# Kernel tuning notes

Measured on AMD Instinct MI355X. Metric: run time of the kernel, lower is better.

The kernel has to match this reference:

```python
import jax, jax.numpy as jnp
import numpy as np

B, N, F, FE, H, C = 2, 2048, 128, 8, 4, 64
LEAKY_ALPHA = 0.2
NEG_INF = -1e9


def setup_inputs() -> dict:
    key = jax.random.key(0)
    ks = jax.random.split(key, 8)
    return {
        "X": jax.random.normal(ks[0], (B, N, F), jnp.float32),
        "A": jax.random.uniform(ks[1], (B, N, N), jnp.float32),
        "E": jax.random.normal(ks[2], (B, N, N, FE), jnp.float32),
        "W_edge": jax.random.normal(ks[3], (FE, 1), jnp.float32) * 0.1,
        "b_edge": jnp.zeros((1,), jnp.float32),
        "W_gat": jax.random.normal(ks[4], (H, F, C), jnp.float32) * 0.05,
        "a_src": jax.random.normal(ks[5], (H, C), jnp.float32) * 0.1,
        "a_dst": jax.random.normal(ks[6], (H, C), jnp.float32) * 0.1,
        "b_gat": jnp.zeros((H * C,), jnp.float32),
        "ln_gamma": jnp.ones((H * C,), jnp.float32),
        "ln_beta": jnp.zeros((H * C,), jnp.float32),
    }


def reference(X, A, E, W_edge, b_edge, W_gat, a_src, a_dst, b_gat, ln_gamma, ln_beta):
    # --- edge gate: sigmoid(Dense_1(E)) -> [B,N,N], multiply into adjacency ---
    edge_w = jax.nn.sigmoid(jnp.einsum("bije,eo->bijo", E, W_edge) + b_edge)
    A = A * edge_w[..., 0]  # [B,N,N]

    # --- multi-head dense GAT (spektral GATConv, concat_heads, elu) ---
    h = jnp.einsum("bnf,hfc->bnhc", X, W_gat)  # [B,N,H,C]
    s_src = jnp.einsum("bnhc,hc->bnh", h, a_src)  # [B,N,H]
    s_dst = jnp.einsum("bnhc,hc->bnh", h, a_dst)
    # e_ij = LeakyReLU(src_i + dst_j): [B,N(i),N(j),H]
    logits = jax.nn.leaky_relu(s_src[:, :, None, :] + s_dst[:, None, :, :],
                               negative_slope=LEAKY_ALPHA)
    mask = jnp.where(A == 0.0, NEG_INF, 0.0)[..., None]  # [B,N,N,1]
    attn = jax.nn.softmax(logits + mask, axis=2)  # softmax over neighbors j
    out = jnp.einsum("bijh,bjhc->bihc", attn, h)  # [B,N,H,C]
    out = out.reshape(B, N, H * C) + b_gat
    out = jax.nn.elu(out)

    # --- LayerNorm over the feature axis (inference: dropout is identity) ---
    mu = jnp.mean(out, axis=-1, keepdims=True)
    var = jnp.var(out, axis=-1, keepdims=True)
    out = (out - mu) * jax.lax.rsqrt(var + 1e-3) * ln_gamma + ln_beta
    return out
```

## Files before the change

### kernel.cpp

```cpp
#include <hip/hip_runtime.h>
#include <hip/hip_bf16.h>


#define BB 2
#define NN 2048
#define FF 128
#define HH 4
#define CC 64
#define HC 256
#define TN 8
#define LOG2E 1.4426950408889634f

typedef __attribute__((ext_vector_type(8))) short short8;
typedef __attribute__((ext_vector_type(4))) float f32x4;

__device__ __forceinline__ float wave_sum(float v) {
#pragma unroll
    for (int m = 32; m >= 1; m >>= 1) v += __shfl_xor(v, m, 64);
    return v;
}

__device__ __forceinline__ unsigned short bf16rne(float x) {
    unsigned u = __float_as_uint(x);
    return (unsigned short)((u + 0x7fffu + ((u >> 16) & 1u)) >> 16);
}

__global__ __launch_bounds__(256) void k1_proj(
    const float* __restrict__ X, const float* __restrict__ Adj,
    const float* __restrict__ Wg,
    const float* __restrict__ a_src, const float* __restrict__ a_dst,
    unsigned short* __restrict__ hT, float* __restrict__ ssT,
    float* __restrict__ sdT, unsigned char* __restrict__ zT)
{
    __shared__ float sX[TN][FF];
    const int blk = blockIdx.x;
    const int b  = blk / (NN / TN);
    const int n0 = (blk % (NN / TN)) * TN;
    const int tid = threadIdx.x;
    const int h = tid >> 6, c = tid & 63;

    for (int idx = tid; idx < TN * FF; idx += 256) {
        int r = idx >> 7, f = idx & 127;
        sX[r][f] = X[(size_t)(b * NN + n0 + r) * FF + f];
    }
    __syncthreads();

    float hv[TN];
#pragma unroll
    for (int r = 0; r < TN; ++r) hv[r] = 0.f;

#pragma unroll 4
    for (int f4 = 0; f4 < FF / 4; ++f4) {
        const int f = f4 * 4;
        const float w0 = Wg[(h * FF + f + 0) * CC + c];
        const float w1 = Wg[(h * FF + f + 1) * CC + c];
        const float w2 = Wg[(h * FF + f + 2) * CC + c];
        const float w3 = Wg[(h * FF + f + 3) * CC + c];
#pragma unroll
        for (int r = 0; r < TN; ++r) {
            float4 x4 = *(const float4*)&sX[r][f];
            hv[r] = fmaf(x4.x, w0, hv[r]);
            hv[r] = fmaf(x4.y, w1, hv[r]);
            hv[r] = fmaf(x4.z, w2, hv[r]);
            hv[r] = fmaf(x4.w, w3, hv[r]);
        }
    }

    union { short8 v; unsigned short u[8]; } pk;
#pragma unroll
    for (int r = 0; r < TN; ++r) pk.u[r] = bf16rne(hv[r]);
    *(short8*)&hT[((size_t)(b * HH + h) * CC + c) * NN + n0] = pk.v;

    const float as = a_src[tid];
    const float ad = a_dst[tid];
#pragma unroll
    for (int r = 0; r < TN; ++r) {
        const int n = n0 + r;
        float s1 = wave_sum(hv[r] * as);
        float s2 = wave_sum(hv[r] * ad);
        if (c == 0) {
            ssT[(b * HH + h) * NN + n] = s1 * LOG2E;
            sdT[(b * HH + h) * NN + n] = s2 * LOG2E;
        }
    }

    {
        const int r = tid >> 5;
        const int s = tid & 31;
        const size_t row = (size_t)(b * NN + n0 + r);
        const float* ap = Adj + row * NN + s * 64;
        unsigned char* zp = zT + (row << 8);
#pragma unroll
        for (int k = 0; k < 8; ++k) {
            float4 a0 = *(const float4*)(ap + k * 8);
            float4 a1 = *(const float4*)(ap + k * 8 + 4);
            unsigned m = 0u;
            m |= (a0.x == 0.f) ? 1u   : 0u;
            m |= (a0.y == 0.f) ? 2u   : 0u;
            m |= (a0.z == 0.f) ? 4u   : 0u;
            m |= (a0.w == 0.f) ? 8u   : 0u;
            m |= (a1.x == 0.f) ? 16u  : 0u;
            m |= (a1.y == 0.f) ? 32u  : 0u;
            m |= (a1.z == 0.f) ? 64u  : 0u;
            m |= (a1.w == 0.f) ? 128u : 0u;
            const int jb = s * 8 + k;
            const int jq = jb >> 6, rem = jb & 63;
            const int it = rem >> 2, lq = rem & 3;
            zp[jq * 64 + lq * 16 + it] = (unsigned char)m;
        }
    }
}

struct Stage {
    float4 sda, sdb;
    short8 bfr[4];
};

__device__ __forceinline__ void load_stage(
    Stage& s, const float* sdp, const unsigned short* const* hb, int js)
{
    s.sda = *(const float4*)(sdp + js);
    s.sdb = *(const float4*)(sdp + js + 4);
#pragma unroll
    for (int ni = 0; ni < 4; ++ni) s.bfr[ni] = *(const short8*)(hb[ni] + js);
}

__device__ __forceinline__ void consume_stage(
    const Stage& s, float ss, unsigned mb, float& lsum, f32x4* acc)
{
    const float sd[8] = {s.sda.x, s.sda.y, s.sda.z, s.sda.w,
                         s.sdb.x, s.sdb.y, s.sdb.z, s.sdb.w};
    float p[8];
#pragma unroll
    for (int t = 0; t < 8; ++t) {
        float x = ss + sd[t];
        x = fmaxf(x, 0.2f * x);
        p[t] = __builtin_amdgcn_exp2f(x);
    }
    if (mb) {
#pragma unroll
        for (int t = 0; t < 8; ++t)
            if ((mb >> t) & 1u) p[t] = 0.f;
    }
#pragma unroll
    for (int t = 0; t < 8; ++t) lsum += p[t];

    union { short8 v; __hip_bfloat162 h2[4]; } pk;
#pragma unroll
    for (int t = 0; t < 4; ++t)
        pk.h2[t] = __float22bfloat162_rn(make_float2(p[2 * t], p[2 * t + 1]));
#pragma unroll
    for (int ni = 0; ni < 4; ++ni)
        acc[ni] = __builtin_amdgcn_mfma_f32_16x16x32_bf16(pk.v, s.bfr[ni], acc[ni], 0, 0, 0);
}

__global__ __launch_bounds__(1024, 4) void k2_attn(
    const unsigned short* __restrict__ hT, const float* __restrict__ ssT,
    const float* __restrict__ sdT, const unsigned char* __restrict__ zT,
    const float* __restrict__ b_gat, const float* __restrict__ gamma,
    const float* __restrict__ beta, float* __restrict__ out)
{
    __shared__ float accs[3][16][HH][64];
    __shared__ float lsumx[3][HH][16];
    __shared__ float red1s[HH][16], red2s[HH][16];

    const int blk = blockIdx.x;
    const int b  = blk >> 7;
    const int i0 = (blk & 127) << 4;
    const int tid  = threadIdx.x;
    const int wave = tid >> 6;
    const int h  = wave & 3;
    const int jq = wave >> 2;
    const int l  = tid & 63;
    const int lr = l & 15;
    const int lq = l >> 4;

    const float ss = ssT[(b * HH + h) * NN + i0 + lr];

    const uint4 mw = *(const uint4*)(zT + ((size_t)(b * NN + i0 + lr) << 8)
                                       + jq * 64 + lq * 16);
    const unsigned long long mlo = ((unsigned long long)mw.y << 32) | mw.x;
    const unsigned long long mhi = ((unsigned long long)mw.w << 32) | mw.z;

    f32x4 acc[4];
#pragma unroll
    for (int ni = 0; ni < 4; ++ni) acc[ni] = (f32x4){0.f, 0.f, 0.f, 0.f};
    float lsum = 0.f;

    const float* sdp  = sdT + (b * HH + h) * NN + jq * 512 + lq * 8;
    const unsigned short* hb[4];
#pragma unroll
    for (int ni = 0; ni < 4; ++ni)
        hb[ni] = hT + ((size_t)(b * HH + h) * CC + ni * 16 + lr) * NN + jq * 512 + lq * 8;

    Stage s0, s1;
    load_stage(s0, sdp, hb, 0);
#pragma unroll 2
    for (int it = 0; it < 16; it += 2) {
        const unsigned long long msel = (it & 8) ? mhi : mlo;
        const int sh = (it & 7) * 8;
        const unsigned mb0 = (unsigned)(msel >> sh) & 0xffu;
        const unsigned mb1 = (unsigned)(msel >> (sh + 8)) & 0xffu;
        load_stage(s1, sdp, hb, (it + 1) * 32);
        consume_stage(s0, ss, mb0, lsum, acc);
        if (it + 2 < 16) load_stage(s0, sdp, hb, (it + 2) * 32);
        consume_stage(s1, ss, mb1, lsum, acc);
    }

    lsum += __shfl_xor(lsum, 16, 64);
    lsum += __shfl_xor(lsum, 32, 64);

    if (jq > 0) {
        if (lq == 0) lsumx[jq - 1][h][lr] = lsum;
#pragma unroll
        for (int ni = 0; ni < 4; ++ni)
#pragma unroll
            for (int r = 0; r < 4; ++r)
                accs[jq - 1][ni * 4 + r][h][l] = acc[ni][r];
    }
    __syncthreads();

    if (jq == 0) {
        const float lcomb = lsum + lsumx[0][h][lr] + lsumx[1][h][lr] + lsumx[2][h][lr];
        float lrow[4];
#pragma unroll
        for (int r = 0; r < 4; ++r) lrow[r] = __shfl(lcomb, lq * 4 + r, 64);

        float bg[4];
#pragma unroll
        for (int ni = 0; ni < 4; ++ni) bg[ni] = b_gat[h * 64 + ni * 16 + lr];

        float vals[4][4];
        float s1[4] = {0.f, 0.f, 0.f, 0.f}, s2[4] = {0.f, 0.f, 0.f, 0.f};
#pragma unroll
        for (int ni = 0; ni < 4; ++ni)
#pragma unroll
            for (int r = 0; r < 4; ++r) {
                float a = acc[ni][r] + accs[0][ni * 4 + r][h][l]
                        + accs[1][ni * 4 + r][h][l] + accs[2][ni * 4 + r][h][l];
                float v = a / lrow[r] + bg[ni];
                v = (v > 0.f) ? v : (__expf(v) - 1.f);
                vals[ni][r] = v;
                s1[r] += v;
                s2[r] += v * v;
            }
#pragma unroll
        for (int m = 1; m <= 8; m <<= 1)
#pragma unroll
            for (int r = 0; r < 4; ++r) {
                s1[r] += __shfl_xor(s1[r], m, 64);
                s2[r] += __shfl_xor(s2[r], m, 64);
            }
        if (lr == 0)
#pragma unroll
            for (int r = 0; r < 4; ++r) {
                red1s[h][lq * 4 + r] = s1[r];
                red2s[h][lq * 4 + r] = s2[r];
            }
        __syncthreads();

        const float gm[4] = {gamma[h * 64 + lr], gamma[h * 64 + 16 + lr],
                             gamma[h * 64 + 32 + lr], gamma[h * 64 + 48 + lr]};
        const float bm[4] = {beta[h * 64 + lr], beta[h * 64 + 16 + lr],
                             beta[h * 64 + 32 + lr], beta[h * 64 + 48 + lr]};
#pragma unroll
        for (int r = 0; r < 4; ++r) {
            const int row = lq * 4 + r;
            float S1 = red1s[0][row] + red1s[1][row] + red1s[2][row] + red1s[3][row];
            float S2 = red2s[0][row] + red2s[1][row] + red2s[2][row] + red2s[3][row];
            float mu  = S1 * (1.f / HC);
            float var = S2 * (1.f / HC) - mu * mu;
            float inv = rsqrtf(var + 1e-3f);
            float* op = out + (size_t)(b * NN + i0 + row) * HC + h * 64 + lr;
#pragma unroll
            for (int ni = 0; ni < 4; ++ni)
                op[ni * 16] = (vals[ni][r] - mu) * inv * gm[ni] + bm[ni];
        }
    } else {
        __syncthreads();
    }
}

extern "C" void kernel_launch(void* const* d_in, const int* in_sizes, int n_in,
                              void* d_out, int out_size, void* d_ws, size_t ws_size,
                              hipStream_t stream)
{
    const float* X     = (const float*)d_in[0];
    const float* Adj   = (const float*)d_in[1];
    const float* Wg    = (const float*)d_in[5];
    const float* a_src = (const float*)d_in[6];
    const float* a_dst = (const float*)d_in[7];
    const float* b_gat = (const float*)d_in[8];
    const float* gam   = (const float*)d_in[9];
    const float* bet   = (const float*)d_in[10];
    float* out = (float*)d_out;

    const size_t hT_elems = (size_t)BB * HH * CC * NN;
    const size_t ss_elems = (size_t)BB * HH * NN;

    unsigned short* hT = (unsigned short*)d_ws;
    float* ssT = (float*)(hT + hT_elems);
    float* sdT = ssT + ss_elems;
    unsigned char* zT = (unsigned char*)(sdT + ss_elems);

    k1_proj<<<BB * NN / TN, 256, 0, stream>>>(X, Adj, Wg, a_src, a_dst, hT, ssT, sdT, zT);
    k2_attn<<<BB * (NN / 16), 1024, 0, stream>>>(hT, ssT, sdT, zT, b_gat, gam, bet, out);
}
```

Baseline: 380.7 us.

## Block hT into 8-node chunks for contiguous MFMA B-operand loads

Changes the hT layout from [b,h,c,n] to [b,h,n/8,c,8], so each wave's four B-fragment loads per stage come from one base pointer with small fixed offsets instead of four rows strided by N. The projection kernel now reads X straight from global memory instead of staging it in shared memory. The attention loop switches to a two-stage prefetch with unroll 1, and the mask select and row-sum are folded into the exp loop. The aim is better coalescing and fewer address registers, at the cost of uncached repeated X reads in k1 and possibly less latency hiding from the smaller unroll.

```diff
diff --git a/kernel.cpp b/kernel.cpp
--- a/kernel.cpp
+++ b/kernel.cpp
@@ -9,6 +9,7 @@
 #define CC 64
 #define HC 256
 #define TN 8
+#define JB (NN / 8)
 #define LOG2E 1.4426950408889634f
 
 typedef __attribute__((ext_vector_type(8))) short short8;
@@ -32,22 +33,17 @@
     unsigned short* __restrict__ hT, float* __restrict__ ssT,
     float* __restrict__ sdT, unsigned char* __restrict__ zT)
 {
-    __shared__ float sX[TN][FF];
     const int blk = blockIdx.x;
     const int b  = blk / (NN / TN);
     const int n0 = (blk % (NN / TN)) * TN;
     const int tid = threadIdx.x;
     const int h = tid >> 6, c = tid & 63;
 
-    for (int idx = tid; idx < TN * FF; idx += 256) {
-        int r = idx >> 7, f = idx & 127;
-        sX[r][f] = X[(size_t)(b * NN + n0 + r) * FF + f];
-    }
-    __syncthreads();
-
     float hv[TN];
 #pragma unroll
     for (int r = 0; r < TN; ++r) hv[r] = 0.f;
+
+    const float* xp = X + (size_t)(b * NN + n0) * FF;
 
 #pragma unroll 4
     for (int f4 = 0; f4 < FF / 4; ++f4) {
@@ -58,7 +54,7 @@
         const float w3 = Wg[(h * FF + f + 3) * CC + c];
 #pragma unroll
         for (int r = 0; r < TN; ++r) {
-            float4 x4 = *(const float4*)&sX[r][f];
+            float4 x4 = *(const float4*)(xp + r * FF + f);
             hv[r] = fmaf(x4.x, w0, hv[r]);
             hv[r] = fmaf(x4.y, w1, hv[r]);
             hv[r] = fmaf(x4.z, w2, hv[r]);
@@ -69,7 +65,7 @@
     union { short8 v; unsigned short u[8]; } pk;
 #pragma unroll
     for (int r = 0; r < TN; ++r) pk.u[r] = bf16rne(hv[r]);
-    *(short8*)&hT[((size_t)(b * HH + h) * CC + c) * NN + n0] = pk.v;
+    *(short8*)&hT[((((size_t)b * HH + h) * JB + (n0 >> 3)) * CC + c) * 8] = pk.v;
 
     const float as = a_src[tid];
     const float ad = a_dst[tid];
@@ -117,12 +113,15 @@
 };
 
 __device__ __forceinline__ void load_stage(
-    Stage& s, const float* sdp, const unsigned short* const* hb, int js)
-{
+    Stage& s, const float* sdp, const unsigned short* hb, int it)
+{
+    const int js = it * 32;
     s.sda = *(const float4*)(sdp + js);
     s.sdb = *(const float4*)(sdp + js + 4);
-#pragma unroll
-    for (int ni = 0; ni < 4; ++ni) s.bfr[ni] = *(const short8*)(hb[ni] + js);
+    const unsigned short* hp = hb + it * 2048;
+#pragma unroll
+    for (int ni = 0; ni < 4; ++ni)
+        s.bfr[ni] = *(const short8*)(hp + ni * 128);
 }
 
 __device__ __forceinline__ void consume_stage(
@@ -135,16 +134,10 @@
     for (int t = 0; t < 8; ++t) {
         float x = ss + sd[t];
         x = fmaxf(x, 0.2f * x);
-        p[t] = __builtin_amdgcn_exp2f(x);
-    }
-    if (mb) {
-#pragma unroll
-        for (int t = 0; t < 8; ++t)
-            if ((mb >> t) & 1u) p[t] = 0.f;
-    }
-#pragma unroll
-    for (int t = 0; t < 8; ++t) lsum += p[t];
-
+        float pv = __builtin_amdgcn_exp2f(x);
+        p[t] = ((mb >> t) & 1u) ? 0.f : pv;
+        lsum += p[t];
+    }
     union { short8 v; __hip_bfloat162 h2[4]; } pk;
 #pragma unroll
     for (int t = 0; t < 4; ++t)
@@ -187,24 +180,23 @@
     for (int ni = 0; ni < 4; ++ni) acc[ni] = (f32x4){0.f, 0.f, 0.f, 0.f};
     float lsum = 0.f;
 
-    const float* sdp  = sdT + (b * HH + h) * NN + jq * 512 + lq * 8;
-    const unsigned short* hb[4];
-#pragma unroll
-    for (int ni = 0; ni < 4; ++ni)
-        hb[ni] = hT + ((size_t)(b * HH + h) * CC + ni * 16 + lr) * NN + jq * 512 + lq * 8;
+    const float* sdp = sdT + (b * HH + h) * NN + jq * 512 + lq * 8;
+    const unsigned short* hb =
+        hT + ((((size_t)b * HH + h) * JB + jq * 64 + lq) * CC + lr) * 8;
 
     Stage s0, s1;
     load_stage(s0, sdp, hb, 0);
-#pragma unroll 2
+    load_stage(s1, sdp, hb, 1);
+#pragma unroll 1
     for (int it = 0; it < 16; it += 2) {
         const unsigned long long msel = (it & 8) ? mhi : mlo;
         const int sh = (it & 7) * 8;
         const unsigned mb0 = (unsigned)(msel >> sh) & 0xffu;
         const unsigned mb1 = (unsigned)(msel >> (sh + 8)) & 0xffu;
-        load_stage(s1, sdp, hb, (it + 1) * 32);
         consume_stage(s0, ss, mb0, lsum, acc);
-        if (it + 2 < 16) load_stage(s0, sdp, hb, (it + 2) * 32);
+        if (it + 2 < 16) load_stage(s0, sdp, hb, it + 2);
         consume_stage(s1, ss, mb1, lsum, acc);
+        if (it + 3 < 16) load_stage(s1, sdp, hb, it + 3);
     }
 
     lsum += __shfl_xor(lsum, 16, 64);
```

Measured after the change: 369.9 us. -2.8%, faster.
